# Kernel optimization log

Hardware: AMD Instinct MI355X
Metric: run time of the kernel (lower is better)

The kernel has to match this reference:

```python
import jax, jax.numpy as jnp
import numpy as np

B, SX, SY, W, M = 256, 179, 15, 26, 7
VR_MEAN, VR_STD = 400.0, 100.0


def _inorm(x, eps=1e-5):
    # InstanceNorm2d(affine=False): normalize over (H, W) per (b, c)
    mu = x.mean(axis=(2, 3), keepdims=True)
    var = x.var(axis=(2, 3), keepdims=True)
    return (x - mu) / jnp.sqrt(var + eps)


def _cplx(w):
    return w[..., 0] + 1j * w[..., 1]


def _spec(x, w1, w2):
    # SpectralConv2d: rfft2 -> mode-truncated complex mix -> irfft2
    xft = jnp.fft.rfft2(x)  # (B, C, SX, SY//2+1)
    o1 = jnp.einsum('bixy,ioxy->boxy', xft[:, :, :M, :M], _cplx(w1))
    o2 = jnp.einsum('bixy,ioxy->boxy', xft[:, :, -M:, :M], _cplx(w2))
    out = jnp.zeros_like(xft)
    out = out.at[:, :, :M, :M].set(o1).at[:, :, -M:, :M].set(o2)
    return jnp.fft.irfft2(out, s=x.shape[-2:])


def _c1(x, w, b):
    # 1x1 Conv2d as channel einsum
    return jnp.einsum('bihw,oi->bohw', x, w) + b[None, :, None, None]


def _mlp(x, w1, b1, w2, b2):
    return _c1(jax.nn.gelu(_c1(x, w1, b1), approximate=False), w2, b2)


def reference(x, p_w, p_b, sc0_w1, sc0_w2, sc1_w1, sc1_w2,
              mlp0_w1, mlp0_b1, mlp0_w2, mlp0_b2,
              mlp1_w1, mlp1_b1, mlp1_w2, mlp1_b2,
              w0_w, w0_b, w1_w, w1_b,
              sa_cw, sa_cb, sa_fw, sa_fb,
              o1_w1, o1_b1, o1_w2, o1_b2, reg2_w, reg2_b):
    b = x.shape[0]
    x0 = (x[:, :128, -1] - VR_MEAN) / VR_STD  # (B, 128)
    u = x[:, :, :-1][..., None]               # (B, SX, SY, 1)
    gx = jnp.broadcast_to(jnp.linspace(0.0, 1.0, SX, dtype=x.dtype).reshape(1, SX, 1, 1), (b, SX, SY, 1))
    gy = jnp.broadcast_to(jnp.linspace(0.0, 1.0, SY, dtype=x.dtype).reshape(1, 1, SY, 1), (b, SX, SY, 1))
    u = jnp.concatenate([u, gx, gy], axis=-1)  # (B, SX, SY, 3)
    h = jnp.einsum('bxyc,wc->bwxy', u, p_w) + p_b[None, :, None, None]  # (B, W, SX, SY)
    # two Fourier blocks: gelu(mlp(norm(spec(norm(h)))) + w(h))
    h = jax.nn.gelu(_mlp(_inorm(_spec(_inorm(h), sc0_w1, sc0_w2)), mlp0_w1, mlp0_b1, mlp0_w2, mlp0_b2)
                    + _c1(h, w0_w, w0_b), approximate=False)
    h = jax.nn.gelu(_mlp(_inorm(_spec(_inorm(h), sc1_w1, sc1_w2)), mlp1_w1, mlp1_b1, mlp1_w2, mlp1_b2)
                    + _c1(h, w1_w, w1_b), approximate=False)
    # spatial attention: conv3x3 -> relu -> global avg pool -> fc -> sigmoid
    a = jax.lax.conv_general_dilated(h, sa_cw, (1, 1), ((1, 1), (1, 1)),
                                     dimension_numbers=('NCHW', 'OIHW', 'NCHW')) + sa_cb[None, :, None, None]
    a = jax.nn.relu(a).mean(axis=(2, 3))           # (B, W)
    a = jax.nn.sigmoid(a @ sa_fw.T + sa_fb)        # (B, 1)
    h = h * a[:, :, None, None]
    flat = h.reshape(b, -1)                        # (B, 69810)
    x1 = jax.nn.leaky_relu(flat @ o1_w1.T + o1_b1) @ o1_w2.T + o1_b2  # (B, 128)
    z = jnp.stack([x1, x0], axis=-1).reshape(b, -1)  # vstack+permute+reshape -> (B, 256)
    return (z @ reg2_w.T + reg2_b).squeeze(-1)       # (B,)


def setup_inputs() -> dict:
    key = jax.random.key(0)
    ks = jax.random.split(key, 32)
    f32 = jnp.float32
    nrm = lambda i, shp, s=0.02: jax.random.normal(ks[i], shp, dtype=f32) * s
    scale = 1.0 / (W * W)
    uni = lambda i: jax.random.uniform(ks[i], (W, W, M, M, 2), dtype=f32) * scale
    return dict(
        x=jax.random.normal(ks[0], (B, SX, SY + 1), dtype=f32),
        p_w=nrm(1, (W, 3), 0.3), p_b=jnp.zeros((W,), f32),
        sc0_w1=uni(2), sc0_w2=uni(3), sc1_w1=uni(4), sc1_w2=uni(5),
        mlp0_w1=nrm(6, (W, W)), mlp0_b1=jnp.zeros((W,), f32),
        mlp0_w2=nrm(7, (W, W)), mlp0_b2=jnp.zeros((W,), f32),
        mlp1_w1=nrm(8, (W, W)), mlp1_b1=jnp.zeros((W,), f32),
        mlp1_w2=nrm(9, (W, W)), mlp1_b2=jnp.zeros((W,), f32),
        w0_w=nrm(10, (W, W)), w0_b=jnp.zeros((W,), f32),
        w1_w=nrm(11, (W, W)), w1_b=jnp.zeros((W,), f32),
        sa_cw=nrm(12, (W, W, 3, 3)), sa_cb=jnp.zeros((W,), f32),
        sa_fw=nrm(13, (1, W)), sa_fb=jnp.zeros((1,), f32),
        o1_w1=nrm(14, (2808, W * SX * SY), 0.003), o1_b1=jnp.zeros((2808,), f32),
        o1_w2=nrm(15, (128, 2808)), o1_b2=jnp.zeros((128,), f32),
        reg2_w=nrm(16, (1, 256)), reg2_b=jnp.zeros((1,), f32),
    )
```

## Files before the change

### kernel.cpp

```cpp
#include <hip/hip_runtime.h>

typedef __attribute__((ext_vector_type(8))) short short8;
typedef __attribute__((ext_vector_type(4))) float floatx4;

#define SXc 179
#define SYc 15
#define SPc 2685
#define WCH 26
#define CHWc 69810
#define N1c 2808
#define KPADc 69824L

__device__ __forceinline__ float geluf(float x){
  return 0.5f*x*(1.f + erff(x*0.7071067811865475f));
}
__device__ __forceinline__ unsigned short f2bfu(float f){
  unsigned int u = __float_as_uint(f);
  u = (u + 0x7fffu + ((u>>16)&1u)) >> 16;
  return (unsigned short)u;
}

__global__ void k_zero(float* p, int n){
  int i = blockIdx.x*256 + threadIdx.x;
  if (i < n) p[i] = 0.f;
}

__global__ __launch_bounds__(256) void k_embed(const float* __restrict__ xin,
    const float* __restrict__ pw, const float* __restrict__ pb, float* __restrict__ Hg){
  int idx = blockIdx.x*256 + threadIdx.x;
  int b = idx / CHWc; int r = idx - b*CHWc;
  int c = r / SPc;    int p = r - c*SPc;
  int x = p / 15;     int y = p - x*15;
  float u0 = xin[(b*SXc + x)*16 + y];
  float gx = x*(1.f/178.f), gy = y*(1.f/14.f);
  Hg[idx] = u0*pw[c*3] + gx*pw[c*3+1] + gy*pw[c*3+2] + pb[c];
}

__global__ __launch_bounds__(256) void k_fwd_dft(const float* __restrict__ Hg, float* __restrict__ Fg){
  __shared__ float sh[SPc];
  __shared__ float2 fy[SXc*7];
  __shared__ float2 part[392];
  __shared__ float2 t179[SXc];
  __shared__ float2 t15[SYc];
  __shared__ float red[8];
  const int tid = threadIdx.x;
  const int bc = blockIdx.x;
  const float* hp = Hg + (size_t)bc*SPc;
  for (int j = tid; j < SXc; j += 256){ float s,c; sincosf(6.283185307179586f*j*(1.f/179.f), &s, &c); t179[j] = make_float2(c,s); }
  for (int j = tid; j < SYc; j += 256){ float s,c; sincosf(6.283185307179586f*j*(1.f/15.f), &s, &c); t15[j] = make_float2(c,s); }
  float s1 = 0.f, s2 = 0.f;
  for (int i = tid; i < SPc; i += 256){ float v = hp[i]; sh[i] = v; s1 += v; s2 += v*v; }
  #pragma unroll
  for (int off=32; off>0; off>>=1){ s1 += __shfl_down(s1,off); s2 += __shfl_down(s2,off); }
  if ((tid&63)==0){ red[tid>>6] = s1; red[4+(tid>>6)] = s2; }
  __syncthreads();
  s1 = red[0]+red[1]+red[2]+red[3];
  s2 = red[4]+red[5]+red[6]+red[7];
  const float mean = s1*(1.f/SPc);
  const float inv = rsqrtf(s2*(1.f/SPc) - mean*mean + 1e-5f);
  for (int i = tid; i < SPc; i += 256) sh[i] = (sh[i]-mean)*inv;
  __syncthreads();
  for (int t = tid; t < SXc*7; t += 256){
    int x = t/7, ky = t - x*7;
    float re=0.f, im=0.f;
    const float* hb = sh + x*15;
    for (int y=0;y<15;y++){
      float v = hb[y];
      float2 w = t15[(ky*y)%15];
      re = fmaf(v,  w.x, re);
      im = fmaf(-v, w.y, im);
    }
    fy[t] = make_float2(re, im);
  }
  __syncthreads();
  for (int t = tid; t < 392; t += 256){
    int o = t>>2, q = t&3;
    int kxi = o/7, ky = o - kxi*7;
    int kx = (kxi<7) ? kxi : kxi+165;
    int x0 = q*45, x1e = (x0+45 < SXc) ? x0+45 : SXc;
    float re=0.f, im=0.f;
    for (int x=x0;x<x1e;x++){
      float2 f = fy[x*7+ky];
      float2 w = t179[(kx*x)%179];
      re += f.x*w.x + f.y*w.y;
      im += f.y*w.x - f.x*w.y;
    }
    part[t] = make_float2(re, im);
  }
  __syncthreads();
  const int b = bc/WCH, ch = bc - (bc/WCH)*WCH;
  for (int t = tid; t < 98; t += 256){
    float2 a0=part[4*t], a1=part[4*t+1], a2=part[4*t+2], a3=part[4*t+3];
    float* outp = Fg + (((size_t)b*98 + t)*WCH + ch)*2;
    outp[0] = a0.x+a1.x+a2.x+a3.x;
    outp[1] = a0.y+a1.y+a2.y+a3.y;
  }
}

__global__ __launch_bounds__(256) void k_mix(const float* __restrict__ Fg, float* __restrict__ F2g,
                      const float* __restrict__ w1, const float* __restrict__ w2){
  const int b = blockIdx.x, tid = threadIdx.x;
  __shared__ float2 fin[98*WCH];
  const float2* src = (const float2*)(Fg + (size_t)b*98*WCH*2);
  for (int i = tid; i < 98*WCH; i += 256) fin[i] = src[i];
  __syncthreads();
  for (int t = tid; t < 98*WCH; t += 256){
    int pos = t/WCH, o = t - pos*WCH;
    int kxi = pos/7, ky = pos - kxi*7;
    const float* wsrc = (kxi<7) ? w1 : w2;
    int mx = (kxi<7) ? kxi : kxi-7;
    float re=0.f, im=0.f;
    const float2* fp = fin + pos*WCH;
    for (int i=0;i<WCH;i++){
      float2 f = fp[i];
      const float* wp = wsrc + (((i*WCH+o)*7+mx)*7+ky)*2;
      float wr = wp[0], wi = wp[1];
      re += f.x*wr - f.y*wi;
      im += f.x*wi + f.y*wr;
    }
    float2* dst = (float2*)(F2g + (((size_t)b*WCH + o)*98 + pos)*2);
    *dst = make_float2(re, im);
  }
}

__global__ __launch_bounds__(256) void k_inv_dft(const float* __restrict__ F2g, float* __restrict__ Tg){
  __shared__ float2 fin[98];
  __shared__ float2 tmp[SXc*7];
  __shared__ float outv[SPc];
  __shared__ float2 t179[SXc];
  __shared__ float2 t15[SYc];
  __shared__ float red[8];
  const int tid = threadIdx.x;
  const int bc = blockIdx.x;
  for (int j = tid; j < SXc; j += 256){ float s,c; sincosf(6.283185307179586f*j*(1.f/179.f), &s, &c); t179[j] = make_float2(c,s); }
  for (int j = tid; j < SYc; j += 256){ float s,c; sincosf(6.283185307179586f*j*(1.f/15.f), &s, &c); t15[j] = make_float2(c,s); }
  const float2* src = (const float2*)(F2g + (size_t)bc*98*2);
  for (int j = tid; j < 98; j += 256) fin[j] = src[j];
  __syncthreads();
  for (int t = tid; t < SXc*7; t += 256){
    int x = t/7, ky = t - (t/7)*7;
    float re=0.f, im=0.f;
    #pragma unroll
    for (int kxi=0;kxi<14;kxi++){
      float2 f = fin[kxi*7+ky];
      int kx = (kxi<7) ? kxi : kxi+165;
      float2 w = t179[(kx*x)%179];
      re += f.x*w.x - f.y*w.y;
      im += f.x*w.y + f.y*w.x;
    }
    tmp[t] = make_float2(re, im);
  }
  __syncthreads();
  float s1=0.f, s2=0.f;
  for (int p = tid; p < SPc; p += 256){
    int x = p/15, y = p - x*15;
    const float2* tp = tmp + x*7;
    float v = tp[0].x;
    #pragma unroll
    for (int ky=1;ky<7;ky++){
      float2 f = tp[ky];
      float2 w = t15[(ky*y)%15];
      v += 2.f*(f.x*w.x - f.y*w.y);
    }
    v *= (1.f/2685.f);
    outv[p] = v; s1 += v; s2 += v*v;
  }
  #pragma unroll
  for (int off=32; off>0; off>>=1){ s1 += __shfl_down(s1,off); s2 += __shfl_down(s2,off); }
  if ((tid&63)==0){ red[tid>>6] = s1; red[4+(tid>>6)] = s2; }
  __syncthreads();
  s1 = red[0]+red[1]+red[2]+red[3];
  s2 = red[4]+red[5]+red[6]+red[7];
  const float mean = s1*(1.f/SPc);
  const float inv = rsqrtf(s2*(1.f/SPc) - mean*mean + 1e-5f);
  float* outp = Tg + (size_t)bc*SPc;
  for (int p = tid; p < SPc; p += 256) outp[p] = (outv[p]-mean)*inv;
}

__global__ __launch_bounds__(256) void k_mlp_res(const float* __restrict__ Tg, float* __restrict__ Hg,
     const float* __restrict__ w1, const float* __restrict__ b1,
     const float* __restrict__ w2, const float* __restrict__ b2,
     const float* __restrict__ ww, const float* __restrict__ wb){
  const int idx = blockIdx.x*256 + threadIdx.x;
  const int b = idx / SPc, p = idx - (idx/SPc)*SPc;
  const float* tp = Tg + (size_t)b*CHWc + p;
  float* hp = Hg + (size_t)b*CHWc + p;
  float tv[WCH], hv[WCH], m1[WCH];
  #pragma unroll
  for (int i=0;i<WCH;i++) tv[i] = tp[i*SPc];
  #pragma unroll
  for (int i=0;i<WCH;i++) hv[i] = hp[i*SPc];
  #pragma unroll
  for (int o=0;o<WCH;o++){
    float a = b1[o];
    #pragma unroll
    for (int i=0;i<WCH;i++) a = fmaf(tv[i], w1[o*WCH+i], a);
    m1[o] = geluf(a);
  }
  #pragma unroll
  for (int o=0;o<WCH;o++){
    float a = b2[o] + wb[o];
    #pragma unroll
    for (int i=0;i<WCH;i++) a = fmaf(m1[i], w2[o*WCH+i], a);
    #pragma unroll
    for (int i=0;i<WCH;i++) a = fmaf(hv[i], ww[o*WCH+i], a);
    hp[o*SPc] = geluf(a);
  }
}

__global__ __launch_bounds__(256) void k_conv_att(const float* __restrict__ Hg, float* __restrict__ Sg,
                           const float* __restrict__ cw, const float* __restrict__ cb){
  const int b = blockIdx.y;
  const int p = blockIdx.x*256 + threadIdx.x;
  const bool valid = (p < SPc);
  const int x = p/15, y = p - (p/15)*15;
  float acc[WCH];
  #pragma unroll
  for (int o=0;o<WCH;o++) acc[o] = 0.f;
  const float* hb = Hg + (size_t)b*CHWc;
  for (int i=0;i<WCH;i++){
    const float* hc = hb + i*SPc;
    #pragma unroll
    for (int dx=0;dx<3;dx++){
      const int xx = x + dx - 1;
      #pragma unroll
      for (int dy=0;dy<3;dy++){
        const int yy = y + dy - 1;
        float v = 0.f;
        if (valid && xx>=0 && xx<SXc && yy>=0 && yy<SYc) v = hc[xx*15+yy];
        #pragma unroll
        for (int o=0;o<WCH;o++) acc[o] = fmaf(v, cw[((o*WCH+i)*3+dx)*3+dy], acc[o]);
      }
    }
  }
  #pragma unroll
  for (int o=0;o<WCH;o++){
    float r = valid ? fmaxf(acc[o] + cb[o], 0.f) : 0.f;
    #pragma unroll
    for (int off=32; off>0; off>>=1) r += __shfl_down(r, off);
    if ((threadIdx.x&63)==0) atomicAdd(&Sg[b*WCH+o], r);
  }
}

__global__ void k_attfc(const float* __restrict__ Sg, const float* __restrict__ fw,
                        const float* __restrict__ fb, float* __restrict__ Ag){
  int b = threadIdx.x;
  float a = fb[0];
  for (int o=0;o<WCH;o++) a = fmaf(Sg[b*WCH+o]*(1.f/2685.f), fw[o], a);
  Ag[b] = 1.f/(1.f + expf(-a));
}

__global__ __launch_bounds__(256) void k_prepA(const float* __restrict__ Hg, unsigned short* __restrict__ Ab){
  int idx = blockIdx.x*256 + threadIdx.x;
  int b = idx / (int)KPADc; int j = idx - b*(int)KPADc;
  float v = (j < CHWc) ? Hg[(size_t)b*CHWc + j] : 0.f;
  Ab[idx] = f2bfu(v);
}

__global__ __launch_bounds__(256) void k_gemm1(const unsigned short* __restrict__ Ab,
                        const float* __restrict__ Wg, float* __restrict__ Cg){
  __shared__ __align__(16) unsigned short As[256*32];
  __shared__ __align__(16) unsigned short Bs[64*32];
  const int tid = threadIdx.x;
  const int bn = blockIdx.x, bs = blockIdx.y;
  const int itStart = bs*91;
  const int itEnd = (itStart+91 < 2182) ? itStart+91 : 2182;
  floatx4 acc[4][4];
  #pragma unroll
  for (int i=0;i<4;i++)
    #pragma unroll
    for (int j=0;j<4;j++){ acc[i][j].x=0.f; acc[i][j].y=0.f; acc[i][j].z=0.f; acc[i][j].w=0.f; }
  const int wave = tid>>6, lane = tid&63;
  const int wm = wave*64;
  const int r16 = lane&15, quad = lane>>4;
  for (int it = itStart; it < itEnd; ++it){
    const int k0 = it*32;
    #pragma unroll
    for (int rr=0; rr<4; rr++){
      int cc = tid + rr*256;
      int row = cc>>2, c16 = cc&3;
      const int4* src = (const int4*)(Ab + (size_t)row*KPADc + (k0 + c16*8));
      ((int4*)As)[cc] = *src;
    }
    #pragma unroll
    for (int rr=0; rr<2; rr++){
      int cc = tid + rr*256;
      int row = cc>>3, c4 = cc&7;
      int n = bn*64 + row;
      int k = k0 + c4*4;
      float v0=0.f,v1=0.f,v2=0.f,v3=0.f;
      if (n < N1c){
        const float* wp = Wg + (size_t)n*CHWc + k;
        if (k+4 <= CHWc){
          const float2* w2p = (const float2*)wp;
          float2 lo = w2p[0], hi = w2p[1];
          v0=lo.x; v1=lo.y; v2=hi.x; v3=hi.y;
        } else {
          if (k   < CHWc) v0 = wp[0];
          if (k+1 < CHWc) v1 = wp[1];
          if (k+2 < CHWc) v2 = wp[2];
          if (k+3 < CHWc) v3 = wp[3];
        }
      }
      ushort4 pk; pk.x=f2bfu(v0); pk.y=f2bfu(v1); pk.z=f2bfu(v2); pk.w=f2bfu(v3);
      ((ushort4*)Bs)[cc] = pk;
    }
    __syncthreads();
    short8 af[4], bf[4];
    #pragma unroll
    for (int t=0;t<4;t++){
      af[t] = *(const short8*)(As + (wm + t*16 + r16)*32 + quad*8);
      bf[t] = *(const short8*)(Bs + (t*16 + r16)*32 + quad*8);
    }
    #pragma unroll
    for (int tm=0;tm<4;tm++)
      #pragma unroll
      for (int tn=0;tn<4;tn++)
        acc[tm][tn] = __builtin_amdgcn_mfma_f32_16x16x32_bf16(af[tm], bf[tn], acc[tm][tn], 0, 0, 0);
    __syncthreads();
  }
  #pragma unroll
  for (int tm=0;tm<4;tm++){
    #pragma unroll
    for (int tn=0;tn<4;tn++){
      int gn = bn*64 + tn*16 + r16;
      if (gn < N1c){
        #pragma unroll
        for (int r=0;r<4;r++){
          int gm = wm + tm*16 + quad*4 + r;
          atomicAdd(&Cg[(size_t)gm*N1c + gn], acc[tm][tn][r]);
        }
      }
    }
  }
}

__global__ __launch_bounds__(128) void k_x1(const float* __restrict__ x1pre, const float* __restrict__ Ag,
                     const float* __restrict__ b1, const float* __restrict__ w2,
                     const float* __restrict__ b2, float* __restrict__ X1){
  const int b = blockIdx.x;
  const int tid = threadIdx.x;
  __shared__ float lr[N1c];
  const float ab = Ag[b];
  for (int n = tid; n < N1c; n += 128){
    float v = fmaf(ab, x1pre[(size_t)b*N1c + n], b1[n]);
    lr[n] = v > 0.f ? v : 0.01f*v;
  }
  __syncthreads();
  float acc = b2[tid];
  const floatx4* wr = (const floatx4*)(w2 + (size_t)tid*N1c);
  const floatx4* l4 = (const floatx4*)lr;
  for (int n=0;n<N1c/4;n++){
    floatx4 w = wr[n], l = l4[n];
    acc += l.x*w.x + l.y*w.y + l.z*w.z + l.w*w.w;
  }
  X1[b*128 + tid] = acc;
}

__global__ void k_final(const float* __restrict__ X1, const float* __restrict__ xin,
                        const float* __restrict__ rw, const float* __restrict__ rb,
                        float* __restrict__ outp){
  int b = threadIdx.x;
  float acc = rb[0];
  for (int k=0;k<128;k++){
    float x1v = X1[b*128+k];
    float x0v = (xin[(b*SXc + k)*16 + 15] - 400.f)*0.01f;
    acc = fmaf(x1v, rw[2*k], acc);
    acc = fmaf(x0v, rw[2*k+1], acc);
  }
  outp[b] = acc;
}

extern "C" void kernel_launch(void* const* d_in, const int* in_sizes, int n_in,
                              void* d_out, int out_size, void* d_ws, size_t ws_size,
                              hipStream_t stream) {
  const float* xin  = (const float*)d_in[0];
  const float* p_w  = (const float*)d_in[1];
  const float* p_b  = (const float*)d_in[2];
  const float* sc_w1[2] = {(const float*)d_in[3], (const float*)d_in[5]};
  const float* sc_w2[2] = {(const float*)d_in[4], (const float*)d_in[6]};
  const float* m_w1[2]  = {(const float*)d_in[7],  (const float*)d_in[11]};
  const float* m_b1[2]  = {(const float*)d_in[8],  (const float*)d_in[12]};
  const float* m_w2[2]  = {(const float*)d_in[9],  (const float*)d_in[13]};
  const float* m_b2[2]  = {(const float*)d_in[10], (const float*)d_in[14]};
  const float* w_w[2]   = {(const float*)d_in[15], (const float*)d_in[17]};
  const float* w_b[2]   = {(const float*)d_in[16], (const float*)d_in[18]};
  const float* sa_cw = (const float*)d_in[19];
  const float* sa_cb = (const float*)d_in[20];
  const float* sa_fw = (const float*)d_in[21];
  const float* sa_fb = (const float*)d_in[22];
  const float* o1w1  = (const float*)d_in[23];
  const float* o1b1  = (const float*)d_in[24];
  const float* o1w2  = (const float*)d_in[25];
  const float* o1b2  = (const float*)d_in[26];
  const float* rw    = (const float*)d_in[27];
  const float* rb    = (const float*)d_in[28];

  char* ws = (char*)d_ws;
  float* Hb  = (float*)(ws + 0);
  float* Tb  = (float*)(ws + 71485440);
  float* Fb  = (float*)(ws + 142970880);
  float* F2b = (float*)(ws + 148189184);
  unsigned short* Ab = (unsigned short*)(ws + 71485440);
  float* x1pre = (float*)(ws + 142970880);
  float* X1b   = (float*)(ws + 142970880 + 2875392);
  float* Sb    = (float*)(ws + 142970880 + 2875392 + 131072);
  float* Aat   = (float*)(ws + 142970880 + 2875392 + 131072 + 26624);

  k_embed<<<CHWc, 256, 0, stream>>>(xin, p_w, p_b, Hb);

  for (int blk = 0; blk < 2; ++blk){
    k_fwd_dft<<<256*WCH, 256, 0, stream>>>(Hb, Fb);
    k_mix<<<256, 256, 0, stream>>>(Fb, F2b, sc_w1[blk], sc_w2[blk]);
    k_inv_dft<<<256*WCH, 256, 0, stream>>>(F2b, Tb);
    k_mlp_res<<<SPc, 256, 0, stream>>>(Tb, Hb, m_w1[blk], m_b1[blk], m_w2[blk], m_b2[blk], w_w[blk], w_b[blk]);
  }

  k_zero<<<26, 256, 0, stream>>>(Sb, 256*WCH);
  k_conv_att<<<dim3(11, 256), 256, 0, stream>>>(Hb, Sb, sa_cw, sa_cb);
  k_attfc<<<1, 256, 0, stream>>>(Sb, sa_fw, sa_fb, Aat);

  k_prepA<<<(int)KPADc, 256, 0, stream>>>(Hb, Ab);
  k_zero<<<N1c, 256, 0, stream>>>(x1pre, 256*N1c);
  k_gemm1<<<dim3(44, 24), 256, 0, stream>>>(Ab, o1w1, x1pre);
  k_x1<<<256, 128, 0, stream>>>(x1pre, Aat, o1b1, o1w2, o1b2, X1b);
  k_final<<<1, 256, 0, stream>>>(X1b, xin, rw, rb, (float*)d_out);
}
```

Before: 2.951 ms.

## Double-buffer GEMM1 with async LDS loads, swizzle, and larger N tile

Restructures the big activation×weight GEMM. It now double-buffers the A and B shared-memory tiles, using global_load_lds for A and register prefetch of fp32 weights for B, so the next k-step's loads overlap the current MFMAs. It also XOR-swizzles the LDS layout to avoid bank conflicts and widens the block to 512 threads with a 256x128 tile, which halves A re-reads across N blocks. The cost is more shared memory and registers per block, and a different split-K grid (23 slices of 95 iterations).

```diff
diff --git a/kernel.cpp b/kernel.cpp
--- a/kernel.cpp
+++ b/kernel.cpp
@@ -257,77 +257,111 @@
   Ab[idx] = f2bfu(v);
 }
 
-__global__ __launch_bounds__(256) void k_gemm1(const unsigned short* __restrict__ Ab,
+__global__ __launch_bounds__(512, 4) void k_gemm1(const unsigned short* __restrict__ Ab,
                         const float* __restrict__ Wg, float* __restrict__ Cg){
-  __shared__ __align__(16) unsigned short As[256*32];
-  __shared__ __align__(16) unsigned short Bs[64*32];
+  __shared__ __align__(16) unsigned short As[2][256*32];
+  __shared__ __align__(16) unsigned short Bs[2][128*32];
   const int tid = threadIdx.x;
   const int bn = blockIdx.x, bs = blockIdx.y;
-  const int itStart = bs*91;
-  const int itEnd = (itStart+91 < 2182) ? itStart+91 : 2182;
+  const int itStart = bs*95;
+  const int itEnd = (itStart+95 < 2182) ? itStart+95 : 2182;
+  const int wave = tid>>6, lane = tid&63;
+  const int wm = (wave>>1)*64;
+  const int wn = (wave&1)*64;
+  const int r16 = lane&15, quad = lane>>4;
+  const int swz = r16&3;
+
+  const int wrow = tid>>2, wseg0 = tid&3;
+  const int wsegG = wseg0 ^ (wrow&3);
+  const int gn_w = bn*128 + wrow;
+  const bool wvalid = (gn_w < N1c);
+  const float* wbase = Wg + (size_t)gn_w*CHWc;
+
   floatx4 acc[4][4];
   #pragma unroll
   for (int i=0;i<4;i++)
     #pragma unroll
     for (int j=0;j<4;j++){ acc[i][j].x=0.f; acc[i][j].y=0.f; acc[i][j].z=0.f; acc[i][j].w=0.f; }
-  const int wave = tid>>6, lane = tid&63;
-  const int wm = wave*64;
-  const int r16 = lane&15, quad = lane>>4;
+
+  float wv0,wv1,wv2,wv3,wv4,wv5,wv6,wv7;
+
+  auto stageA = [&](int buf, int it){
+    const int k0 = it*32;
+    #pragma unroll
+    for (int i=0;i<2;i++){
+      const int chunk = (i*8 + wave)*64 + lane;
+      const int row = chunk>>2, q = chunk&3;
+      const int qs = q ^ (row&3);
+      const unsigned short* gp = Ab + (size_t)row*KPADc + (k0 + qs*8);
+      unsigned short* lp = &As[buf][(i*8 + wave)*512];
+      __builtin_amdgcn_global_load_lds((__attribute__((address_space(1))) void*)gp,
+                                       (__attribute__((address_space(3))) void*)lp, 16, 0, 0);
+    }
+  };
+  auto loadW = [&](int it){
+    const int kk = it*32 + wsegG*8;
+    if (wvalid && kk + 8 <= CHWc){
+      const float2* p = (const float2*)(wbase + kk);
+      float2 a = p[0], b2_ = p[1], c = p[2], d = p[3];
+      wv0=a.x; wv1=a.y; wv2=b2_.x; wv3=b2_.y; wv4=c.x; wv5=c.y; wv6=d.x; wv7=d.y;
+    } else {
+      wv0 = (wvalid && kk   < CHWc) ? wbase[kk]   : 0.f;
+      wv1 = (wvalid && kk+1 < CHWc) ? wbase[kk+1] : 0.f;
+      wv2 = (wvalid && kk+2 < CHWc) ? wbase[kk+2] : 0.f;
+      wv3 = (wvalid && kk+3 < CHWc) ? wbase[kk+3] : 0.f;
+      wv4 = (wvalid && kk+4 < CHWc) ? wbase[kk+4] : 0.f;
+      wv5 = (wvalid && kk+5 < CHWc) ? wbase[kk+5] : 0.f;
+      wv6 = (wvalid && kk+6 < CHWc) ? wbase[kk+6] : 0.f;
+      wv7 = (wvalid && kk+7 < CHWc) ? wbase[kk+7] : 0.f;
+    }
+  };
+  auto writeW = [&](int buf){
+    short8 pk;
+    pk[0]=(short)f2bfu(wv0); pk[1]=(short)f2bfu(wv1);
+    pk[2]=(short)f2bfu(wv2); pk[3]=(short)f2bfu(wv3);
+    pk[4]=(short)f2bfu(wv4); pk[5]=(short)f2bfu(wv5);
+    pk[6]=(short)f2bfu(wv6); pk[7]=(short)f2bfu(wv7);
+    *(short8*)(&Bs[buf][tid*8]) = pk;
+  };
+
+  loadW(itStart);
+  stageA(0, itStart);
+  writeW(0);
+  __syncthreads();
+
+  int cur = 0;
   for (int it = itStart; it < itEnd; ++it){
-    const int k0 = it*32;
-    #pragma unroll
-    for (int rr=0; rr<4; rr++){
-      int cc = tid + rr*256;
-      int row = cc>>2, c16 = cc&3;
-      const int4* src = (const int4*)(Ab + (size_t)row*KPADc + (k0 + c16*8));
-      ((int4*)As)[cc] = *src;
-    }
-    #pragma unroll
-    for (int rr=0; rr<2; rr++){
-      int cc = tid + rr*256;
-      int row = cc>>3, c4 = cc&7;
-      int n = bn*64 + row;
-      int k = k0 + c4*4;
-      float v0=0.f,v1=0.f,v2=0.f,v3=0.f;
-      if (n < N1c){
-        const float* wp = Wg + (size_t)n*CHWc + k;
-        if (k+4 <= CHWc){
-          const float2* w2p = (const float2*)wp;
-          float2 lo = w2p[0], hi = w2p[1];
-          v0=lo.x; v1=lo.y; v2=hi.x; v3=hi.y;
-        } else {
-          if (k   < CHWc) v0 = wp[0];
-          if (k+1 < CHWc) v1 = wp[1];
-          if (k+2 < CHWc) v2 = wp[2];
-          if (k+3 < CHWc) v3 = wp[3];
-        }
-      }
-      ushort4 pk; pk.x=f2bfu(v0); pk.y=f2bfu(v1); pk.z=f2bfu(v2); pk.w=f2bfu(v3);
-      ((ushort4*)Bs)[cc] = pk;
-    }
-    __syncthreads();
+    const int nxt = cur^1;
+    const bool more = (it+1 < itEnd);
+    if (more){
+      stageA(nxt, it+1);
+      loadW(it+1);
+    }
     short8 af[4], bf[4];
     #pragma unroll
     for (int t=0;t<4;t++){
-      af[t] = *(const short8*)(As + (wm + t*16 + r16)*32 + quad*8);
-      bf[t] = *(const short8*)(Bs + (t*16 + r16)*32 + quad*8);
+      af[t] = *(const short8*)(&As[cur][(wm + t*16 + r16)*32 + ((quad ^ swz)*8)]);
+      bf[t] = *(const short8*)(&Bs[cur][(wn + t*16 + r16)*32 + ((quad ^ swz)*8)]);
     }
     #pragma unroll
     for (int tm=0;tm<4;tm++)
       #pragma unroll
       for (int tn=0;tn<4;tn++)
         acc[tm][tn] = __builtin_amdgcn_mfma_f32_16x16x32_bf16(af[tm], bf[tn], acc[tm][tn], 0, 0, 0);
+    if (more) writeW(nxt);
     __syncthreads();
-  }
+    cur = nxt;
+  }
+
   #pragma unroll
   for (int tm=0;tm<4;tm++){
     #pragma unroll
     for (int tn=0;tn<4;tn++){
-      int gn = bn*64 + tn*16 + r16;
+      const int gn = bn*128 + wn + tn*16 + r16;
       if (gn < N1c){
         #pragma unroll
         for (int r=0;r<4;r++){
-          int gm = wm + tm*16 + quad*4 + r;
+          const int gm = wm + tm*16 + quad*4 + r;
           atomicAdd(&Cg[(size_t)gm*N1c + gn], acc[tm][tn][r]);
         }
       }
@@ -422,7 +456,7 @@
 
   k_prepA<<<(int)KPADc, 256, 0, stream>>>(Hb, Ab);
   k_zero<<<N1c, 256, 0, stream>>>(x1pre, 256*N1c);
-  k_gemm1<<<dim3(44, 24), 256, 0, stream>>>(Ab, o1w1, x1pre);
+  k_gemm1<<<dim3(22, 23), 512, 0, stream>>>(Ab, o1w1, x1pre);
   k_x1<<<256, 128, 0, stream>>>(x1pre, Aat, o1b1, o1w2, o1b2, X1b);
   k_final<<<1, 256, 0, stream>>>(X1b, xin, rw, rb, (float*)d_out);
 }
```

Result: faster. 2.637 ms (-10.6%).
